# Kernel tuning notes

Measured on AMD Instinct MI355X. Metric: run time of the kernel, lower is better.

The kernel has to match this reference:

```python
import jax, jax.numpy as jnp
import numpy as np

ENTITY_SIZE = 500000
DIM = 128
REL_SIZE = 500
EDGE_W_ROWS = REL_SIZE * (REL_SIZE + 1) + 1  # 250501
B = 4096
N = 64


def setup_inputs() -> dict:
    key = jax.random.key(0)
    k1, k2, k3, k4, k5, k6, k7, k8 = jax.random.split(key, 8)
    data_r = jax.random.randint(k1, (B, N), 0, EDGE_W_ROWS, dtype=jnp.int64 if jax.config.jax_enable_x64 else jnp.int32)
    data_e = jax.random.randint(k2, (B, N), 0, ENTITY_SIZE + 1)
    rel = jax.random.randint(k3, (B,), 0, REL_SIZE)
    pos_id = jax.random.randint(k4, (B,), 0, ENTITY_SIZE + 1)
    neg_id = jax.random.randint(k5, (B,), 0, ENTITY_SIZE + 1)
    ent_emb = jax.random.normal(k6, (ENTITY_SIZE + 1, DIM), dtype=jnp.float32)
    edge_w = jax.random.normal(k7, (EDGE_W_ROWS, 1), dtype=jnp.float32)
    rel_emb = jax.random.normal(k8, (REL_SIZE, DIM), dtype=jnp.float32)
    return {"data_r": data_r, "data_e": data_e, "rel": rel, "pos_id": pos_id,
            "neg_id": neg_id, "ent_emb": ent_emb, "edge_w": edge_w, "rel_emb": rel_emb}


def reference(data_r, data_e, rel, pos_id, neg_id, ent_emb, edge_w, rel_emb):
    # edge-weight gather -> [B, N] logits, softmax over neighbors
    w = jax.nn.softmax(edge_w[data_r].reshape(data_e.shape[0], -1), axis=1)  # [B, N]
    e = ent_emb[data_e]                       # [B, N, D] neighbor entity embeddings
    Eh = jnp.sum(e * w[:, :, None], axis=1)   # softmax-weighted sum -> [B, D]
    out_t = Eh + rel_emb[rel]                 # add relation embedding
    pos_out = ent_emb[pos_id]                 # [B, D]
    neg_out = ent_emb[neg_id]                 # [B, D]
    return (out_t, pos_out, neg_out)
```

## Files before the change

### kernel.cpp

```cpp
#include <hip/hip_runtime.h>

#define BB 4096
#define NN 64
#define DD 128

__global__ __launch_bounds__(256) void fused_gather_softmax_agg(
    const int* __restrict__ data_r,
    const int* __restrict__ data_e,
    const int* __restrict__ rel,
    const int* __restrict__ pos_id,
    const int* __restrict__ neg_id,
    const float* __restrict__ ent_emb,
    const float* __restrict__ edge_w,
    const float* __restrict__ rel_emb,
    float* __restrict__ out)
{
    const int wave = threadIdx.x >> 6;
    const int lane = threadIdx.x & 63;
    const int b    = blockIdx.x * 4 + wave;

    const int ridx = data_r[b * NN + lane];
    const float wv = edge_w[ridx];

    float m = wv;
#pragma unroll
    for (int off = 32; off; off >>= 1) m = fmaxf(m, __shfl_xor(m, off));
    const float ex = __expf(wv - m);
    float s = ex;
#pragma unroll
    for (int off = 32; off; off >>= 1) s += __shfl_xor(s, off);
    const float w = ex / s;

    const int eidx = data_e[b * NN + lane];

    const int rg = lane >> 4;
    const int sl = lane & 15;

    float acc[8];
#pragma unroll
    for (int i = 0; i < 8; ++i) acc[i] = 0.f;

#pragma unroll 4
    for (int t = 0; t < 16; ++t) {
        const int   n   = t * 4 + rg;
        const int   idx = __shfl(eidx, n);
        const float wn  = __shfl(w, n);
        const float4* rp = (const float4*)(ent_emb + (size_t)idx * DD) + sl * 2;
        const float4 v0 = rp[0];
        const float4 v1 = rp[1];
        acc[0] = fmaf(wn, v0.x, acc[0]); acc[1] = fmaf(wn, v0.y, acc[1]);
        acc[2] = fmaf(wn, v0.z, acc[2]); acc[3] = fmaf(wn, v0.w, acc[3]);
        acc[4] = fmaf(wn, v1.x, acc[4]); acc[5] = fmaf(wn, v1.y, acc[5]);
        acc[6] = fmaf(wn, v1.z, acc[6]); acc[7] = fmaf(wn, v1.w, acc[7]);
    }

#pragma unroll
    for (int i = 0; i < 8; ++i) {
        acc[i] += __shfl_xor(acc[i], 16);
        acc[i] += __shfl_xor(acc[i], 32);
    }

    if (rg == 0) {
        const int r = rel[b];
        const float4* rv = (const float4*)(rel_emb + (size_t)r * DD) + sl * 2;
        const float4 r0 = rv[0];
        const float4 r1 = rv[1];
        float4 o0, o1;
        o0.x = acc[0] + r0.x; o0.y = acc[1] + r0.y;
        o0.z = acc[2] + r0.z; o0.w = acc[3] + r0.w;
        o1.x = acc[4] + r1.x; o1.y = acc[5] + r1.y;
        o1.z = acc[6] + r1.z; o1.w = acc[7] + r1.w;
        float4* op = (float4*)(out + (size_t)b * DD) + sl * 2;
        op[0] = o0;
        op[1] = o1;
    } else if (rg == 1) {
        const int p = pos_id[b];
        const float4* rp = (const float4*)(ent_emb + (size_t)p * DD) + sl * 2;
        float4* op = (float4*)(out + (size_t)BB * DD + (size_t)b * DD) + sl * 2;
        op[0] = rp[0];
        op[1] = rp[1];
    } else if (rg == 2) {
        const int ng = neg_id[b];
        const float4* rp = (const float4*)(ent_emb + (size_t)ng * DD) + sl * 2;
        float4* op = (float4*)(out + (size_t)2 * BB * DD + (size_t)b * DD) + sl * 2;
        op[0] = rp[0];
        op[1] = rp[1];
    }
}

extern "C" void kernel_launch(void* const* d_in, const int* in_sizes, int n_in,
                              void* d_out, int out_size, void* d_ws, size_t ws_size,
                              hipStream_t stream) {
    const int* data_r = (const int*)d_in[0];
    const int* data_e = (const int*)d_in[1];
    const int* rel    = (const int*)d_in[2];
    const int* pos_id = (const int*)d_in[3];
    const int* neg_id = (const int*)d_in[4];
    const float* ent_emb = (const float*)d_in[5];
    const float* edge_w  = (const float*)d_in[6];
    const float* rel_emb = (const float*)d_in[7];
    float* out = (float*)d_out;

    dim3 grid(BB / 4);
    dim3 block(256);
    fused_gather_softmax_agg<<<grid, block, 0, stream>>>(
        data_r, data_e, rel, pos_id, neg_id, ent_emb, edge_w, rel_emb, out);
}
```

Measured before the change: 330.8 us.

## Split each batch row's neighbor aggregation across four waves with LDS reduction

Each block now handles one batch row instead of four, and the 64 neighbors are split across the four waves, with each wave gathering 16 neighbor rows. Partial sums are combined through shared memory, and the output goes through a coalesced per-dimension store. The float4 loads are rearranged so each row read is contiguous across lanes. The aim is more memory-level parallelism and more blocks in flight. The cost is that every wave redoes the softmax and reloads the index vectors, and a block-wide barrier is added.

```diff
diff --git a/kernel.cpp b/kernel.cpp
--- a/kernel.cpp
+++ b/kernel.cpp
@@ -15,11 +15,14 @@
     const float* __restrict__ rel_emb,
     float* __restrict__ out)
 {
+    __shared__ float part[4 * DD];
+
+    const int b    = blockIdx.x;
     const int wave = threadIdx.x >> 6;
     const int lane = threadIdx.x & 63;
-    const int b    = blockIdx.x * 4 + wave;
 
     const int ridx = data_r[b * NN + lane];
+    const int eidx = data_e[b * NN + lane];
     const float wv = edge_w[ridx];
 
     float m = wv;
@@ -31,8 +34,6 @@
     for (int off = 32; off; off >>= 1) s += __shfl_xor(s, off);
     const float w = ex / s;
 
-    const int eidx = data_e[b * NN + lane];
-
     const int rg = lane >> 4;
     const int sl = lane & 15;
 
@@ -40,14 +41,14 @@
 #pragma unroll
     for (int i = 0; i < 8; ++i) acc[i] = 0.f;
 
-#pragma unroll 4
-    for (int t = 0; t < 16; ++t) {
-        const int   n   = t * 4 + rg;
+#pragma unroll
+    for (int t = 0; t < 4; ++t) {
+        const int   n   = wave * 16 + t * 4 + rg;
         const int   idx = __shfl(eidx, n);
         const float wn  = __shfl(w, n);
-        const float4* rp = (const float4*)(ent_emb + (size_t)idx * DD) + sl * 2;
-        const float4 v0 = rp[0];
-        const float4 v1 = rp[1];
+        const float4* rp = (const float4*)(ent_emb + (size_t)idx * DD);
+        const float4 v0 = rp[sl];
+        const float4 v1 = rp[sl + 16];
         acc[0] = fmaf(wn, v0.x, acc[0]); acc[1] = fmaf(wn, v0.y, acc[1]);
         acc[2] = fmaf(wn, v0.z, acc[2]); acc[3] = fmaf(wn, v0.w, acc[3]);
         acc[4] = fmaf(wn, v1.x, acc[4]); acc[5] = fmaf(wn, v1.y, acc[5]);
@@ -60,31 +61,28 @@
         acc[i] += __shfl_xor(acc[i], 32);
     }
 
-    if (rg == 0) {
+    if (lane < 16) {
+        float* p = part + wave * DD;
+        *(float4*)(p + sl * 4)      = make_float4(acc[0], acc[1], acc[2], acc[3]);
+        *(float4*)(p + 64 + sl * 4) = make_float4(acc[4], acc[5], acc[6], acc[7]);
+    }
+    __syncthreads();
+
+    if (wave == 0) {
         const int r = rel[b];
-        const float4* rv = (const float4*)(rel_emb + (size_t)r * DD) + sl * 2;
-        const float4 r0 = rv[0];
-        const float4 r1 = rv[1];
-        float4 o0, o1;
-        o0.x = acc[0] + r0.x; o0.y = acc[1] + r0.y;
-        o0.z = acc[2] + r0.z; o0.w = acc[3] + r0.w;
-        o1.x = acc[4] + r1.x; o1.y = acc[5] + r1.y;
-        o1.z = acc[6] + r1.z; o1.w = acc[7] + r1.w;
-        float4* op = (float4*)(out + (size_t)b * DD) + sl * 2;
-        op[0] = o0;
-        op[1] = o1;
-    } else if (rg == 1) {
-        const int p = pos_id[b];
-        const float4* rp = (const float4*)(ent_emb + (size_t)p * DD) + sl * 2;
-        float4* op = (float4*)(out + (size_t)BB * DD + (size_t)b * DD) + sl * 2;
-        op[0] = rp[0];
-        op[1] = rp[1];
-    } else if (rg == 2) {
-        const int ng = neg_id[b];
-        const float4* rp = (const float4*)(ent_emb + (size_t)ng * DD) + sl * 2;
-        float4* op = (float4*)(out + (size_t)2 * BB * DD + (size_t)b * DD) + sl * 2;
-        op[0] = rp[0];
-        op[1] = rp[1];
+#pragma unroll
+        for (int h = 0; h < 2; ++h) {
+            const int d = lane + h * 64;
+            const float v = part[d] + part[DD + d] + part[2 * DD + d] + part[3 * DD + d];
+            out[(size_t)b * DD + d] = v + rel_emb[(size_t)r * DD + d];
+        }
+    } else if (wave == 1) {
+        const int is_neg = lane >> 5;
+        const int id = is_neg ? neg_id[b] : pos_id[b];
+        const int q  = lane & 31;
+        const float4 v = ((const float4*)(ent_emb + (size_t)id * DD))[q];
+        float4* op = (float4*)(out + (size_t)BB * DD * (1 + is_neg) + (size_t)b * DD);
+        op[q] = v;
     }
 }
 
@@ -101,7 +99,7 @@
     const float* rel_emb = (const float*)d_in[7];
     float* out = (float*)d_out;
 
-    dim3 grid(BB / 4);
+    dim3 grid(BB);
     dim3 block(256);
     fused_gather_softmax_agg<<<grid, block, 0, stream>>>(
         data_r, data_e, rel, pos_id, neg_id, ent_emb, edge_w, rel_emb, out);
```

Result: no change. 329.6 us (-0.4%).
